# Kernel tuning notes

Hardware: AMD Instinct MI355X
Metric: run time of the kernel (lower is better)

Reference implementation:

```python
import jax, jax.numpy as jnp
import numpy as np

B, T, S, A = 4, 10, 6, 6
HID, L, IMG = 512, 6, 128
NCH = 16  # spatial-softmax channels
_px, _py = np.meshgrid(np.linspace(-1.0, 1.0, IMG), np.linspace(-1.0, 1.0, IMG))
POSX = jnp.asarray(_px.reshape(-1), jnp.float32)
POSY = jnp.asarray(_py.reshape(-1), jnp.float32)


def _conv_relu(x, w, b):
    y = jax.lax.conv_general_dilated(x, w, (1, 1), 'SAME',
                                     dimension_numbers=('NCHW', 'OIHW', 'NCHW'))
    return jax.nn.relu(y + b[None, :, None, None])


def _cnn_ss(x, ws, bs):
    for w, b in zip(ws, bs):
        x = _conv_relu(x, w, b)
    n = x.shape[0]
    attn = jax.nn.softmax(x.reshape(n, NCH, -1), axis=-1)  # (n, 16, H*W)
    ex = attn @ POSX  # (n, 16)
    ey = attn @ POSY
    return jnp.stack([ex, ey], axis=-1).reshape(n, 2 * NCH)  # (n, 32)


def _lstm_cell(x, h, c, wih, whh, bih, bhh):
    g = x @ wih.T + bih + h @ whh.T + bhh
    i, f, gg, o = jnp.split(g, 4, axis=-1)  # torch LSTMCell gate order i,f,g,o
    c2 = jax.nn.sigmoid(f) * c + jax.nn.sigmoid(i) * jnp.tanh(gg)
    h2 = jax.nn.sigmoid(o) * jnp.tanh(c2)
    return h2, c2


def setup_inputs() -> dict:
    key = jax.random.key(0)
    ks = iter(jax.random.split(key, 64))

    def nrm(shape, s=0.05):
        return jax.random.normal(next(ks), shape, dtype=jnp.float32) * s

    inp = {
        'seq_img_main': nrm((B, T, 3, IMG, IMG), 1.0),
        'seq_img_secondary': nrm((B, T, 3, IMG, IMG), 1.0),
        'seq_states': nrm((B, T, S), 1.0),
    }
    chans = [(32, 3), (64, 32), (128, 64), (16, 128)]
    for cam in ('m', 's'):
        for j, (o, ci) in enumerate(chans):
            inp[f'{cam}_w{j}'] = nrm((o, ci, 3, 3))
            inp[f'{cam}_b{j}'] = nrm((o,))
    in0, inr = S + 64, HID + 64  # 70 and 576
    inp['wih0'] = nrm((4 * HID, in0)); inp['whh0'] = nrm((4 * HID, HID))
    inp['bih0'] = nrm((4 * HID,)); inp['bhh0'] = nrm((4 * HID,))
    inp['wih_r'] = nrm((L - 1, 4 * HID, inr)); inp['whh_r'] = nrm((L - 1, 4 * HID, HID))
    inp['bih_r'] = nrm((L - 1, 4 * HID)); inp['bhh_r'] = nrm((L - 1, 4 * HID))
    inp['out_w'] = nrm((A, inr)); inp['out_b'] = nrm((A,))
    return inp


def reference(seq_img_main, seq_img_secondary, seq_states,
              m_w0, m_b0, m_w1, m_b1, m_w2, m_b2, m_w3, m_b3,
              s_w0, s_b0, s_w1, s_b1, s_w2, s_b2, s_w3, s_b3,
              wih0, whh0, bih0, bhh0, wih_r, whh_r, bih_r, bhh_r,
              out_w, out_b):
    b, t = seq_img_main.shape[:2]
    fm = _cnn_ss(seq_img_main.reshape(b * t, 3, IMG, IMG),
                 [m_w0, m_w1, m_w2, m_w3], [m_b0, m_b1, m_b2, m_b3])
    fs = _cnn_ss(seq_img_secondary.reshape(b * t, 3, IMG, IMG),
                 [s_w0, s_w1, s_w2, s_w3], [s_b0, s_b1, s_b2, s_b3])
    img = jnp.concatenate([fm, fs], axis=-1).reshape(b, t, 64)  # (B,T,64)

    h0 = jnp.zeros((L, b, HID), jnp.float32)
    c0 = jnp.zeros((L, b, HID), jnp.float32)

    def step(carry, xt):
        h, c = carry
        st, im = xt  # (B,S), (B,64)
        x = jnp.concatenate([st, im], axis=-1)
        hn, cn = _lstm_cell(x, h[0], c[0], wih0, whh0, bih0, bhh0)
        hs, cs = [hn], [cn]
        for l in range(L - 1):
            x = jnp.concatenate([hs[-1], im], axis=-1)
            hl, cl = _lstm_cell(x, h[l + 1], c[l + 1],
                                wih_r[l], whh_r[l], bih_r[l], bhh_r[l])
            hs.append(hl); cs.append(cl)
        out = jnp.concatenate([hs[-1], im], axis=-1) @ out_w.T + out_b
        return (jnp.stack(hs), jnp.stack(cs)), out

    _, outs = jax.lax.scan(step, (h0, c0),
                           (seq_states.transpose(1, 0, 2), img.transpose(1, 0, 2)))
    return outs.transpose(1, 0, 2)  # (B,T,A)
```

## Files before the change

### kernel.cpp

```cpp
#include <hip/hip_runtime.h>
#include <hip/hip_bf16.h>
#include <math.h>

typedef __hip_bfloat16 bf16;
typedef short bf16x8 __attribute__((ext_vector_type(8)));
typedef float f32x4 __attribute__((ext_vector_type(4)));

static constexpr int HWPX = 16384;

__device__ inline float sigmoidf_(float x) { return 1.0f / (1.0f + expf(-x)); }
__device__ inline float bflo(unsigned u) { return __uint_as_float(u << 16); }
__device__ inline float bfhi(unsigned u) { return __uint_as_float(u & 0xffff0000u); }
__device__ inline int swz(int x) { return (x ^ (x >> 2)) & 3; }

__device__ inline void gll16(const bf16* g, short* l) {
    __builtin_amdgcn_global_load_lds(
        (const __attribute__((address_space(1))) void*)g,
        (__attribute__((address_space(3))) void*)l, 16, 0, 0);
}

__global__ __launch_bounds__(256) void prep_lstm_k(
    const float* __restrict__ wih0, const float* __restrict__ whh0,
    const float* __restrict__ wihr, const float* __restrict__ whhr,
    bf16* __restrict__ d0, bf16* __restrict__ d1,
    bf16* __restrict__ d2, bf16* __restrict__ d3)
{
    const size_t nA = 2048ull * 72, nB = 2048ull * 512;
    const size_t nC = 5ull * 2048 * 576, nD = 5ull * 2048 * 512;
    for (size_t i = blockIdx.x * 256ull + threadIdx.x; i < nA + nB + nC + nD;
         i += (size_t)gridDim.x * 256) {
        if (i < nA) {
            int c = (int)(i % 72), r = (int)(i / 72);
            d0[i] = __float2bfloat16(c < 70 ? wih0[(size_t)r * 70 + c] : 0.f);
        } else if (i < nA + nB) {
            size_t k = i - nA; d1[k] = __float2bfloat16(whh0[k]);
        } else if (i < nA + nB + nC) {
            size_t k = i - nA - nB; d2[k] = __float2bfloat16(wihr[k]);
        } else {
            size_t k = i - nA - nB - nC; d3[k] = __float2bfloat16(whhr[k]);
        }
    }
}

struct ConvW {
    const float* src[8];
    bf16* dst[8];
};

__global__ __launch_bounds__(256) void prep_conv_k(ConvW a)
{
    const int sizes[4] = {3072, 18432, 73728, 18432};
    const int cins[4] = {3, 32, 64, 128};
    const int couts[4] = {32, 64, 128, 16};
    int total = 2 * 113664;
    for (int idx = blockIdx.x * 256 + threadIdx.x; idx < total; idx += gridDim.x * 256) {
        int i = idx, cam = 0;
        if (i >= 113664) { cam = 1; i -= 113664; }
        int layer = 0;
        while (layer < 3 && i >= sizes[layer]) { i -= sizes[layer]; ++layer; }
        const float* w = a.src[cam * 4 + layer];
        bf16* d = a.dst[cam * 4 + layer];
        if (layer == 0) {
            int k = i & 31, co = (i >> 5) & 31, ky = i >> 10;
            int kx = k >> 3, c = k & 7;
            float v = (kx < 3 && c < 3) ? w[((co * 3 + c) * 3 + ky) * 3 + kx] : 0.f;
            d[i] = __float2bfloat16(v);
        } else {
            int CIN = cins[layer], COUT = couts[layer], KC = CIN / 32;
            int e = i & 7;
            int t2 = i >> 3;
            int co = t2 % COUT;
            int t3 = t2 / COUT;
            int q = t3 & 3;
            int t4 = t3 >> 2;
            int kc = t4 % KC;
            int tap = t4 / KC;
            d[i] = __float2bfloat16(w[((size_t)(co * CIN + kc * 32 + q * 8 + e)) * 9 + tap]);
        }
    }
}

__global__ __launch_bounds__(256, 4) void conv01(
    const float* __restrict__ srcm, const float* __restrict__ srcs,
    const bf16* __restrict__ w0m, const bf16* __restrict__ w0s,
    const float* __restrict__ b0m, const float* __restrict__ b0s,
    const bf16* __restrict__ wTm, const bf16* __restrict__ wTs,
    const float* __restrict__ bm, const float* __restrict__ bs,
    bf16* __restrict__ out, int c0)
{
    constexpr int COUT = 64, MW = 2;
    constexpr int SLOTS = 4 * 264;

    const int y0 = (blockIdx.x >> 1) * 2;
    const int x0 = (blockIdx.x & 1) * 64;
    const int cam = blockIdx.y;
    const int img = blockIdx.z;
    const int ci_ = cam * gridDim.z + img;
    const float* inImg = (cam ? srcs : srcm) + (size_t)(c0 + img) * 3 * HWPX;
    const bf16* wT0 = cam ? w0s : w0m;
    const float* bias0 = cam ? b0s : b0m;
    const bf16* wT = cam ? wTs : wTm;
    const float* bias = cam ? bs : bm;
    const int tid = threadIdx.x;
    const int wave = tid >> 6, lane = tid & 63;
    const int wrow = wave >> 1, wm = wave & 1;
    const int q = lane >> 4, n16 = lane & 15;

    __shared__ short smem[SLOTS * 8];
    __shared__ short raw[6 * 68 * 16];

    for (int i = tid; i < SLOTS; i += 256)
        *(bf16x8*)(void*)&smem[i * 8] = (bf16x8)0;

    for (int d = tid; d < 6 * 68; d += 256) {
        int x = d % 68, r = d / 68;
        int yy = y0 - 2 + r, xx = x0 - 2 + x;
        bf16 v8[8];
#pragma unroll
        for (int c = 0; c < 8; ++c) v8[c] = __float2bfloat16(0.f);
        if ((unsigned)yy < 128u && (unsigned)xx < 128u) {
            int o = yy * 128 + xx;
            v8[0] = __float2bfloat16(inImg[o]);
            v8[1] = __float2bfloat16(inImg[HWPX + o]);
            v8[2] = __float2bfloat16(inImg[2 * HWPX + o]);
        }
        *(bf16x8*)(void*)&raw[d * 16] = *(bf16x8*)(void*)v8;
        *(bf16x8*)(void*)&raw[d * 16 + 8] = (bf16x8)0;
    }
    __syncthreads();

    const int co0_ = wm * 16 + n16;
    for (int rp = 0; rp < 4; ++rp) {
        int Y = y0 - 1 + rp;
        if ((unsigned)Y >= 128u) continue;
        for (int xg = wrow; xg < 5; xg += 2) {
            int xt = xg * 16 + n16;
            int xts = xt < 66 ? xt : 65;
            f32x4 a0 = f32x4{0.f, 0.f, 0.f, 0.f};
#pragma unroll
            for (int ky = 0; ky < 3; ++ky) {
                bf16x8 aF = *(const bf16x8*)(const void*)(wT0 +
                    ((size_t)(ky * 32 + co0_) * 32) + q * 8);
                int off = (q < 3) ? ((rp + ky) * 68 + xts + q) * 16
                                  : ((rp + ky) * 68 + xts) * 16 + 8;
                bf16x8 bF = *(const bf16x8*)(const void*)&raw[off];
                a0 = __builtin_amdgcn_mfma_f32_16x16x32_bf16(aF, bF, a0, 0, 0, 0);
            }
            int X = x0 - 1 + xt;
            if (xt < 66 && (unsigned)X < 128u) {
                int cb0 = wm * 16 + q * 4;
                bf16 tmp[4];
#pragma unroll
                for (int r = 0; r < 4; ++r) {
                    float v = a0[r] + bias0[cb0 + r];
                    tmp[r] = __float2bfloat16(v > 0.f ? v : 0.f);
                }
                int g = cb0 >> 3;
                int sbase = (rp * 264 + xt * 4 + (g ^ swz(xt))) * 8 + (q & 1) * 4;
                *reinterpret_cast<uint2*>(&smem[sbase]) = *reinterpret_cast<uint2*>(tmp);
            }
        }
    }
    __syncthreads();

    f32x4 acc[MW][4];
#pragma unroll
    for (int mt = 0; mt < MW; ++mt)
#pragma unroll
        for (int nt = 0; nt < 4; ++nt) acc[mt][nt] = f32x4{0.f, 0.f, 0.f, 0.f};

#pragma unroll
    for (int ky = 0; ky < 3; ++ky) {
#pragma unroll
        for (int kx = 0; kx < 3; ++kx) {
            bf16x8 aF[MW];
#pragma unroll
            for (int mt = 0; mt < MW; ++mt) {
                int co = (wm * MW + mt) * 16 + n16;
                aF[mt] = *(const bf16x8*)(const void*)(wT +
                    (((size_t)(ky * 3 + kx) * 4 + q) * COUT + co) * 8);
            }
#pragma unroll
            for (int nt = 0; nt < 4; ++nt) {
                int xt = nt * 16 + n16 + kx;
                int slot = (wrow + ky) * 264 + xt * 4 + (q ^ swz(xt));
                bf16x8 bF = *(const bf16x8*)(const void*)&smem[slot * 8];
#pragma unroll
                for (int mt = 0; mt < MW; ++mt)
                    acc[mt][nt] = __builtin_amdgcn_mfma_f32_16x16x32_bf16(
                        aF[mt], bF, acc[mt][nt], 0, 0, 0);
            }
        }
    }

    const int y = y0 + wrow;
#pragma unroll
    for (int mt = 0; mt < MW; ++mt) {
        int co0 = (wm * MW + mt) * 16 + q * 4;
#pragma unroll
        for (int nt = 0; nt < 4; ++nt) {
            int x = x0 + nt * 16 + n16;
            bf16 tmp[4];
#pragma unroll
            for (int r = 0; r < 4; ++r) {
                float v = acc[mt][nt][r] + bias[co0 + r];
                tmp[r] = __float2bfloat16(v > 0.f ? v : 0.f);
            }
            *reinterpret_cast<uint2*>(out + ((size_t)ci_ * HWPX + y * 128 + x) * COUT + co0)
                = *reinterpret_cast<uint2*>(tmp);
        }
    }
}

template <int CIN, int COUT>
__global__ __launch_bounds__(256, 4) void conv2r(
    const bf16* __restrict__ in, const bf16* __restrict__ wTm,
    const bf16* __restrict__ wTs, const float* __restrict__ bm,
    const float* __restrict__ bs, bf16* __restrict__ out,
    const char* __restrict__ zpage)
{
    constexpr int KC = CIN / 32;
    constexpr int NB = (KC > 1) ? 2 : 1;
    constexpr int MW = COUT / 32;
    constexpr int SLOTS = 4 * 264;

    const int y0 = (blockIdx.x >> 1) * 2;
    const int x0 = (blockIdx.x & 1) * 64;
    const int cam = blockIdx.y;
    const int img = blockIdx.z;
    const int ci_ = cam * gridDim.z + img;
    const bf16* wT = cam ? wTs : wTm;
    const float* bias = cam ? bs : bm;
    const int tid = threadIdx.x;
    const int wave = tid >> 6, lane = tid & 63;
    const int wrow = wave >> 1, wm = wave & 1;
    const int q = lane >> 4, n16 = lane & 15;

    __shared__ short smem[NB][SLOTS * 8];
    const bf16* inImg = in + (size_t)ci_ * HWPX * CIN;

    const bf16* sptr[5];
#pragma unroll
    for (int it = 0; it < 5; ++it) {
        int s = it * 256 + tid;
        int r = s / 264, s2 = s - r * 264;
        int sx = s2 >> 2;
        int g = (s2 & 3) ^ swz(sx);
        int yy = y0 + r - 1, xx = x0 + sx - 1;
        bool ok = (s < SLOTS) && ((unsigned)yy < 128u) && ((unsigned)xx < 128u);
        sptr[it] = ok ? inImg + ((size_t)yy * 128 + xx) * CIN + g * 8
                      : (const bf16*)(zpage + (tid & 255) * 16);
    }
    auto stage = [&](int kc, int buf) {
#pragma unroll
        for (int it = 0; it < 5; ++it) {
            if (it * 256 + tid < SLOTS)
                gll16(sptr[it] + kc * 32, &smem[buf][it * 2048 + wave * 512]);
        }
    };

    f32x4 acc[MW][4];
#pragma unroll
    for (int mt = 0; mt < MW; ++mt)
#pragma unroll
        for (int nt = 0; nt < 4; ++nt) acc[mt][nt] = f32x4{0.f, 0.f, 0.f, 0.f};

    stage(0, 0);
    for (int kc = 0; kc < KC; ++kc) {
        __syncthreads();
        if (kc + 1 < KC) stage(kc + 1, (kc + 1) % NB);
        const short* sb = smem[kc % NB];
#pragma unroll
        for (int ky = 0; ky < 3; ++ky) {
#pragma unroll
            for (int kx = 0; kx < 3; ++kx) {
                bf16x8 aF[MW];
#pragma unroll
                for (int mt = 0; mt < MW; ++mt) {
                    int co = (wm * MW + mt) * 16 + n16;
                    aF[mt] = *(const bf16x8*)(const void*)(wT +
                        ((((size_t)(ky * 3 + kx) * KC + kc) * 4 + q) * COUT + co) * 8);
                }
#pragma unroll
                for (int nt = 0; nt < 4; ++nt) {
                    int xt = nt * 16 + n16 + kx;
                    int slot = (wrow + ky) * 264 + xt * 4 + (q ^ swz(xt));
                    bf16x8 bF = *(const bf16x8*)(const void*)&sb[slot * 8];
#pragma unroll
                    for (int mt = 0; mt < MW; ++mt)
                        acc[mt][nt] = __builtin_amdgcn_mfma_f32_16x16x32_bf16(
                            aF[mt], bF, acc[mt][nt], 0, 0, 0);
                }
            }
        }
    }

    const int y = y0 + wrow;
#pragma unroll
    for (int mt = 0; mt < MW; ++mt) {
        int co0 = (wm * MW + mt) * 16 + q * 4;
#pragma unroll
        for (int nt = 0; nt < 4; ++nt) {
            int x = x0 + nt * 16 + n16;
            bf16 tmp[4];
#pragma unroll
            for (int r = 0; r < 4; ++r) {
                float v = acc[mt][nt][r] + bias[co0 + r];
                tmp[r] = __float2bfloat16(v > 0.f ? v : 0.f);
            }
            *reinterpret_cast<uint2*>(out + ((size_t)ci_ * HWPX + y * 128 + x) * COUT + co0)
                = *reinterpret_cast<uint2*>(tmp);
        }
    }
}

__global__ __launch_bounds__(256, 2) void conv4_r4(
    const bf16* __restrict__ in, const bf16* __restrict__ wTm,
    const bf16* __restrict__ wTs, const float* __restrict__ bm,
    const float* __restrict__ bs,
    float* __restrict__ partial,
    const char* __restrict__ zpage, int c0)
{
    constexpr int CIN = 128, KC = 4;
    constexpr int RR = 4;
    constexpr int SLOTS = (RR + 2) * 264;
    const int y0 = (blockIdx.x >> 1) * RR;
    const int xh = blockIdx.x & 1;
    const int x0 = xh * 64;
    const int cam = blockIdx.y;
    const int img = blockIdx.z;
    const int ci_ = cam * gridDim.z + img;
    const int gimg = cam * 40 + c0 + img;
    const bf16* wT = cam ? wTs : wTm;
    const float* bias = cam ? bs : bm;
    const int tid = threadIdx.x;
    const int wave = tid >> 6, lane = tid & 63;
    const int q = lane >> 4, n16 = lane & 15;

    __shared__ short smem[2][SLOTS * 8];
    __shared__ float sred[3][RR][4][16];
    const bf16* inImg = in + (size_t)ci_ * HWPX * CIN;

    const bf16* sptr[7];
#pragma unroll
    for (int it = 0; it < 7; ++it) {
        int s = it * 256 + tid;
        int r = s / 264, s2 = s - r * 264;
        int sx = s2 >> 2;
        int g = (s2 & 3) ^ swz(sx);
        int yy = y0 + r - 1, xx = x0 + sx - 1;
        bool ok = (s < SLOTS) && ((unsigned)yy < 128u) && ((unsigned)xx < 128u);
        sptr[it] = ok ? inImg + ((size_t)yy * 128 + xx) * CIN + g * 8
                      : (const bf16*)(zpage + (tid & 255) * 16);
    }
    auto stage = [&](int kc, int buf) {
#pragma unroll
        for (int it = 0; it < 7; ++it) {
            if (it * 256 + tid < SLOTS)
                gll16(sptr[it] + kc * 32, &smem[buf][it * 2048 + wave * 512]);
        }
    };

    f32x4 acc[RR];
#pragma unroll
    for (int rp = 0; rp < RR; ++rp) acc[rp] = f32x4{0.f, 0.f, 0.f, 0.f};

    stage(0, 0);
    for (int kc = 0; kc < KC; ++kc) {
        __syncthreads();
        if (kc + 1 < KC) stage(kc + 1, (kc + 1) & 1);
        const short* sb = smem[kc & 1];
#pragma unroll
        for (int ky = 0; ky < 3; ++ky) {
#pragma unroll
            for (int kx = 0; kx < 3; ++kx) {
                bf16x8 aF = *(const bf16x8*)(const void*)(wT +
                    ((((size_t)(ky * 3 + kx) * KC + kc) * 4 + q) * 16 + n16) * 8);
                int xt = wave * 16 + n16 + kx;
                int sbase = xt * 4 + (q ^ swz(xt));
#pragma unroll
                for (int rp = 0; rp < RR; ++rp) {
                    bf16x8 bF = *(const bf16x8*)(const void*)
                        &sb[((rp + ky) * 264 + sbase) * 8];
                    acc[rp] = __builtin_amdgcn_mfma_f32_16x16x32_bf16(
                        aF, bF, acc[rp], 0, 0, 0);
                }
            }
        }
    }

    int x = x0 + wave * 16 + n16;
    float px = -1.f + (2.f / 127.f) * x;
    float v[RR][4], M[RR][4];
#pragma unroll
    for (int rp = 0; rp < RR; ++rp)
#pragma unroll
        for (int r = 0; r < 4; ++r) {
            float t = acc[rp][r] + bias[q * 4 + r];
            v[rp][r] = t > 0.f ? t : 0.f;
            M[rp][r] = v[rp][r];
        }
#pragma unroll
    for (int rp = 0; rp < RR; ++rp)
#pragma unroll
        for (int r = 0; r < 4; ++r) {
            M[rp][r] = fmaxf(M[rp][r], __shfl_xor(M[rp][r], 1));
            M[rp][r] = fmaxf(M[rp][r], __shfl_xor(M[rp][r], 2));
            M[rp][r] = fmaxf(M[rp][r], __shfl_xor(M[rp][r], 4));
            M[rp][r] = fmaxf(M[rp][r], __shfl_xor(M[rp][r], 8));
        }
    if (n16 == 0)
#pragma unroll
        for (int rp = 0; rp < RR; ++rp)
#pragma unroll
            for (int r = 0; r < 4; ++r) sred[0][rp][wave][q * 4 + r] = M[rp][r];
    __syncthreads();
#pragma unroll
    for (int rp = 0; rp < RR; ++rp)
#pragma unroll
        for (int r = 0; r < 4; ++r) {
            M[rp][r] = fmaxf(fmaxf(sred[0][rp][0][q * 4 + r], sred[0][rp][1][q * 4 + r]),
                             fmaxf(sred[0][rp][2][q * 4 + r], sred[0][rp][3][q * 4 + r]));
        }
    float s[RR][4], sx[RR][4];
#pragma unroll
    for (int rp = 0; rp < RR; ++rp)
#pragma unroll
        for (int r = 0; r < 4; ++r) {
            float e = expf(v[rp][r] - M[rp][r]);
            s[rp][r] = e; sx[rp][r] = e * px;
            s[rp][r] += __shfl_xor(s[rp][r], 1);  sx[rp][r] += __shfl_xor(sx[rp][r], 1);
            s[rp][r] += __shfl_xor(s[rp][r], 2);  sx[rp][r] += __shfl_xor(sx[rp][r], 2);
            s[rp][r] += __shfl_xor(s[rp][r], 4);  sx[rp][r] += __shfl_xor(sx[rp][r], 4);
            s[rp][r] += __shfl_xor(s[rp][r], 8);  sx[rp][r] += __shfl_xor(sx[rp][r], 8);
        }
    __syncthreads();
    if (n16 == 0)
#pragma unroll
        for (int rp = 0; rp < RR; ++rp)
#pragma unroll
            for (int r = 0; r < 4; ++r) {
                sred[1][rp][wave][q * 4 + r] = s[rp][r];
                sred[2][rp][wave][q * 4 + r] = sx[rp][r];
            }
    __syncthreads();
    if (tid < 16 * RR) {
        int rp = tid >> 4, c = tid & 15;
        float S = sred[1][rp][0][c] + sred[1][rp][1][c] + sred[1][rp][2][c] + sred[1][rp][3][c];
        float SX = sred[2][rp][0][c] + sred[2][rp][1][c] + sred[2][rp][2][c] + sred[2][rp][3][c];
        float Mv = fmaxf(fmaxf(sred[0][rp][0][c], sred[0][rp][1][c]),
                         fmaxf(sred[0][rp][2][c], sred[0][rp][3][c]));
        float* pp = partial + (((size_t)gimg * 16 + c) * 256 + ((y0 + rp) * 2 + xh)) * 4;
        pp[0] = Mv; pp[1] = S; pp[2] = SX;
    }
}

__global__ __launch_bounds__(256) void ssmerge_k(
    const float* __restrict__ partial, float* __restrict__ featm,
    float* __restrict__ feats)
{
    const int img = blockIdx.x;
    const int cam = img / 40, li = img % 40;
    float* feat = cam ? feats : featm;
    const int tid = threadIdx.x;
    const int co = tid >> 4, s = tid & 15;
    const float* base = partial + ((size_t)img * 16 + co) * 256 * 4;
    float M = -1e30f, S = 0.f, SX = 0.f, SY = 0.f;
    for (int i = s; i < 256; i += 16) {
        float m = base[i * 4], sv = base[i * 4 + 1], sxv = base[i * 4 + 2];
        float py = -1.f + (2.f / 127.f) * (i >> 1);
        float Mn = fmaxf(M, m);
        float w0 = expf(M - Mn), w1 = expf(m - Mn);
        S = S * w0 + sv * w1;
        SX = SX * w0 + sxv * w1;
        SY = SY * w0 + sv * py * w1;
        M = Mn;
    }
#pragma unroll
    for (int mask = 1; mask < 16; mask <<= 1) {
        float Mo = __shfl_xor(M, mask), So = __shfl_xor(S, mask);
        float SXo = __shfl_xor(SX, mask), SYo = __shfl_xor(SY, mask);
        float Mn = fmaxf(M, Mo);
        float w0 = expf(M - Mn), w1 = expf(Mo - Mn);
        S = S * w0 + So * w1; SX = SX * w0 + SXo * w1; SY = SY * w0 + SYo * w1;
        M = Mn;
    }
    if (s == 0) {
        feat[(size_t)li * 32 + 2 * co] = SX / S;
        feat[(size_t)li * 32 + 2 * co + 1] = SY / S;
    }
}

__device__ inline float imgfeat(const float* featm, const float* feats,
                                int b, int t, int k)
{
    int idx = (b * 10 + t) * 32;
    return k < 32 ? featm[idx + k] : feats[idx + k - 32];
}

template <int NB1>
__device__ inline void cell_mm(const bf16* __restrict__ wih,
                               const bf16* __restrict__ whh,
                               const float* __restrict__ xs0,
                               int j, int sub, float (&dg)[4][4])
{
    constexpr int K1 = NB1 * 8;
    constexpr int XS = K1 + 512;
#pragma unroll
    for (int r = 0; r < 4; ++r) {
        const uint4* __restrict__ w1 =
            reinterpret_cast<const uint4*>(wih + (size_t)(j + r * 512) * K1);
#pragma unroll
        for (int g0 = 0; g0 < NB1; g0 += 8) {
            int g = g0 + sub;
            if (g0 + 7 < NB1 || g < NB1) {
                uint4 u = w1[g];
                float a0 = bflo(u.x), a1 = bfhi(u.x), a2 = bflo(u.y), a3 = bfhi(u.y);
                float a4 = bflo(u.z), a5 = bfhi(u.z), a6 = bflo(u.w), a7 = bfhi(u.w);
#pragma unroll
                for (int b = 0; b < 4; ++b) {
                    const float* xp = xs0 + b * XS + g * 8;
                    dg[r][b] += a0 * xp[0] + a1 * xp[1] + a2 * xp[2] + a3 * xp[3]
                              + a4 * xp[4] + a5 * xp[5] + a6 * xp[6] + a7 * xp[7];
                }
            }
        }
        const uint4* __restrict__ w2 =
            reinterpret_cast<const uint4*>(whh + (size_t)(j + r * 512) * 512);
#pragma unroll
        for (int gi = 0; gi < 8; ++gi) {
            int g = gi * 8 + sub;
            uint4 u = w2[g];
            float a0 = bflo(u.x), a1 = bfhi(u.x), a2 = bflo(u.y), a3 = bfhi(u.y);
            float a4 = bflo(u.z), a5 = bfhi(u.z), a6 = bflo(u.w), a7 = bfhi(u.w);
#pragma unroll
            for (int b = 0; b < 4; ++b) {
                const float* xp = xs0 + b * XS + K1 + g * 8;
                dg[r][b] += a0 * xp[0] + a1 * xp[1] + a2 * xp[2] + a3 * xp[3]
                          + a4 * xp[4] + a5 * xp[5] + a6 * xp[6] + a7 * xp[7];
            }
        }
    }
}

template <int NB1>
__device__ inline void cell_step(
    int l, int t, int bx,
    const bf16* __restrict__ wih, const bf16* __restrict__ whh,
    const float* __restrict__ bih, const float* __restrict__ bhh,
    const float* __restrict__ states,
    const float* __restrict__ featm, const float* __restrict__ feats,
    float* __restrict__ hAll, float* __restrict__ cst,
    float* __restrict__ xs)
{
    constexpr int K1 = NB1 * 8;
    constexpr int XS = K1 + 512;
    const int tid = threadIdx.x;
    const int jloc = tid >> 3;
    const int sub = tid & 7;
    const int j = bx * 32 + jloc;

    const float* hprev = (l == 0) ? nullptr
                       : hAll + ((size_t)(t + 1) * 6 + (l - 1)) * 2048;
    const float* hold  = hAll + ((size_t)t * 6 + l) * 2048;
    float* hnew        = hAll + ((size_t)(t + 1) * 6 + l) * 2048;

    if (NB1 == 72) {
        for (int i = tid; i < 4 * 512; i += 256) {
            int bb = i >> 9, kk = i & 511;
            float2 cv;
            int base;
            if (kk < 256) {
                cv = *reinterpret_cast<const float2*>(&hprev[bb * 512 + kk * 2]);
                base = bb * XS + kk * 2;
            } else {
                cv = *reinterpret_cast<const float2*>(&hold[bb * 512 + (kk - 256) * 2]);
                base = bb * XS + 576 + (kk - 256) * 2;
            }
            xs[base] = cv.x; xs[base + 1] = cv.y;
        }
        {
            int bb = tid >> 6, k = tid & 63;
            xs[bb * XS + 512 + k] = imgfeat(featm, feats, bb, t, k);
        }
    } else {
        for (int i = tid; i < 4 * 256; i += 256) {
            int bb = i >> 8, kk = i & 255;
            float2 cv = *reinterpret_cast<const float2*>(&hold[bb * 512 + kk * 2]);
            int base = bb * XS + 72 + kk * 2;
            xs[base] = cv.x; xs[base + 1] = cv.y;
        }
        for (int i = tid; i < 4 * 72; i += 256) {
            int bb = i / 72, k = i - bb * 72;
            float v = (k < 6) ? states[(bb * 10 + t) * 6 + k]
                              : (k < 70 ? imgfeat(featm, feats, bb, t, k - 6) : 0.f);
            xs[bb * XS + k] = v;
        }
    }
    __syncthreads();

    float dg[4][4] = {{0.f, 0.f, 0.f, 0.f}, {0.f, 0.f, 0.f, 0.f},
                      {0.f, 0.f, 0.f, 0.f}, {0.f, 0.f, 0.f, 0.f}};
    cell_mm<NB1>(wih, whh, xs, j, sub, dg);

#pragma unroll
    for (int r = 0; r < 4; ++r)
#pragma unroll
        for (int b = 0; b < 4; ++b) {
            dg[r][b] += __shfl_xor(dg[r][b], 1);
            dg[r][b] += __shfl_xor(dg[r][b], 2);
            dg[r][b] += __shfl_xor(dg[r][b], 4);
        }

    if (sub == 0) {
        float b0 = bih[j] + bhh[j];
        float b1 = bih[j + 512] + bhh[j + 512];
        float b2 = bih[j + 1024] + bhh[j + 1024];
        float b3 = bih[j + 1536] + bhh[j + 1536];
#pragma unroll
        for (int b = 0; b < 4; ++b) {
            float gi = dg[0][b] + b0;
            float gf = dg[1][b] + b1;
            float gg = dg[2][b] + b2;
            float go = dg[3][b] + b3;
            float cp = cst[b * 512 + j];
            float c2 = sigmoidf_(gf) * cp + sigmoidf_(gi) * tanhf(gg);
            float h2 = sigmoidf_(go) * tanhf(c2);
            cst[b * 512 + j] = c2;
            hnew[b * 512 + j] = h2;
        }
    }
}

__global__ __launch_bounds__(256) void lstm_diag2_k(
    const bf16* __restrict__ wih0p, const bf16* __restrict__ whh0b,
    const bf16* __restrict__ wihrb, const bf16* __restrict__ whhrb,
    const float* __restrict__ bih0, const float* __restrict__ bhh0,
    const float* __restrict__ bihr, const float* __restrict__ bhhr,
    const float* __restrict__ states,
    const float* __restrict__ featm, const float* __restrict__ feats,
    float* __restrict__ hAll, float* __restrict__ cAll,
    const float* __restrict__ out_w, const float* __restrict__ out_b,
    float* __restrict__ out, int d)
{
    const int l = blockIdx.y;
    const int bx = blockIdx.x;
    const int tid = threadIdx.x;
    __shared__ float xs[4 * 1088];

    if (l == 6) {
        int t = d - 6;
        if (t < 0 || t >= 10 || bx != 0) return;
        const float* h5 = hAll + ((size_t)(t + 1) * 6 + 5) * 2048;
        int p = tid >> 3, sub = tid & 7;
        if (p >= 24) return;
        int b = p / 6, a = p % 6;
        const float* wr = out_w + a * 576;
        float acc = 0.f;
        for (int k = sub; k < 256; k += 8) {
            float2 cv = *reinterpret_cast<const float2*>(&h5[b * 512 + k * 2]);
            acc += wr[k * 2] * cv.x + wr[k * 2 + 1] * cv.y;
        }
        for (int k = sub; k < 64; k += 8)
            acc += wr[512 + k] * imgfeat(featm, feats, b, t, k);
        acc += __shfl_xor(acc, 1);
        acc += __shfl_xor(acc, 2);
        acc += __shfl_xor(acc, 4);
        if (sub == 0) out[(b * 10 + t) * 6 + a] = acc + out_b[a];
        return;
    }

    const int t = d - l;
    if (t < 0 || t >= 10) return;

    float* cst = cAll + (size_t)l * 2048;
    if (l == 0) {
        cell_step<9>(0, t, bx, wih0p, whh0b, bih0, bhh0,
                     states, featm, feats, hAll, cst, xs);
    } else {
        const bf16* wih = wihrb + (size_t)(l - 1) * 2048 * 576;
        const bf16* whh = whhrb + (size_t)(l - 1) * 2048 * 512;
        const float* bih = bihr + (l - 1) * 2048;
        const float* bhh = bhhr + (l - 1) * 2048;
        cell_step<72>(l, t, bx, wih, whh, bih, bhh,
                      states, featm, feats, hAll, cst, xs);
    }
}

extern "C" void kernel_launch(void* const* d_in, const int* in_sizes, int n_in,
                              void* d_out, int out_size, void* d_ws, size_t ws_size,
                              hipStream_t stream)
{
    const float* seq_m = (const float*)d_in[0];
    const float* seq_s = (const float*)d_in[1];
    const float* states = (const float*)d_in[2];
    const float *cw[2][4], *cb[2][4];
    for (int cam = 0; cam < 2; ++cam)
        for (int j = 0; j < 4; ++j) {
            cw[cam][j] = (const float*)d_in[3 + cam * 8 + j * 2];
            cb[cam][j] = (const float*)d_in[3 + cam * 8 + j * 2 + 1];
        }
    const float* wih0  = (const float*)d_in[19];
    const float* whh0  = (const float*)d_in[20];
    const float* bih0  = (const float*)d_in[21];
    const float* bhh0  = (const float*)d_in[22];
    const float* wih_r = (const float*)d_in[23];
    const float* whh_r = (const float*)d_in[24];
    const float* bih_r = (const float*)d_in[25];
    const float* bhh_r = (const float*)d_in[26];
    const float* out_w = (const float*)d_in[27];
    const float* out_b = (const float*)d_in[28];
    float* out = (float*)d_out;

    char* wsc = (char*)d_ws;
    auto carve = [&](size_t bytes) {
        char* p = wsc;
        wsc += (bytes + 255) & ~(size_t)255;
        return p;
    };
    float* featm = (float*)carve(40 * 32 * 4);
    float* feats = (float*)carve(40 * 32 * 4);
    float* hAll  = (float*)carve((size_t)11 * 6 * 2048 * 4);
    float* cAll  = (float*)carve((size_t)6 * 2048 * 4);
    char*  zpage = carve(8192);
    float* partial = (float*)carve((size_t)80 * 16 * 256 * 4 * 4);
    const int wtElts[4] = {3072, 18432, 73728, 18432};
    bf16* wT[2][4];
    for (int cam = 0; cam < 2; ++cam)
        for (int j = 0; j < 4; ++j) wT[cam][j] = (bf16*)carve(wtElts[j] * 2);
    bf16* wih0p = (bf16*)carve((size_t)2048 * 72 * 2);
    bf16* whh0b = (bf16*)carve((size_t)2048 * 512 * 2);
    bf16* wihrb = (bf16*)carve((size_t)5 * 2048 * 576 * 2);
    bf16* whhrb = (bf16*)carve((size_t)5 * 2048 * 512 * 2);

    size_t used = (size_t)(wsc - (char*)d_ws);
    size_t rem = ws_size > used ? ws_size - used : 0;
    int CHI = 1;
    const int cands[8] = {40, 20, 10, 8, 5, 4, 2, 1};
    for (int i = 0; i < 8; ++i) {
        size_t need = (size_t)2 * cands[i] * (128 + 64) * HWPX * 2;
        if (need <= rem) { CHI = cands[i]; break; }
    }
    bf16* bufA = (bf16*)carve((size_t)2 * CHI * HWPX * 128 * 2);
    bf16* bufB = (bf16*)carve((size_t)2 * CHI * HWPX * 64 * 2);

    hipMemsetAsync(hAll, 0, 6 * 2048 * 4, stream);
    hipMemsetAsync(cAll, 0, 6 * 2048 * 4, stream);
    hipMemsetAsync(zpage, 0, 8192, stream);

    prep_lstm_k<<<2048, 256, 0, stream>>>(wih0, whh0, wih_r, whh_r,
                                          wih0p, whh0b, wihrb, whhrb);
    ConvW cwArg;
    for (int cam = 0; cam < 2; ++cam)
        for (int j = 0; j < 4; ++j) {
            cwArg.src[cam * 4 + j] = cw[cam][j];
            cwArg.dst[cam * 4 + j] = wT[cam][j];
        }
    prep_conv_k<<<888, 256, 0, stream>>>(cwArg);

    for (int c0 = 0; c0 < 40; c0 += CHI) {
        int ch = (40 - c0) < CHI ? (40 - c0) : CHI;
        conv01<<<dim3(128, 2, ch), 256, 0, stream>>>(
            seq_m, seq_s, wT[0][0], wT[1][0], cb[0][0], cb[1][0],
            wT[0][1], wT[1][1], cb[0][1], cb[1][1], bufB, c0);
        conv2r<64, 128><<<dim3(128, 2, ch), 256, 0, stream>>>(
            bufB, wT[0][2], wT[1][2], cb[0][2], cb[1][2], bufA, zpage);
        conv4_r4<<<dim3(64, 2, ch), 256, 0, stream>>>(
            bufA, wT[0][3], wT[1][3], cb[0][3], cb[1][3], partial, zpage, c0);
    }
    ssmerge_k<<<80, 256, 0, stream>>>(partial, featm, feats);

    for (int d = 0; d < 16; ++d) {
        lstm_diag2_k<<<dim3(16, 7), 256, 0, stream>>>(
            wih0p, whh0b, wihrb, whhrb, bih0, bhh0, bih_r, bhh_r,
            states, featm, feats, hAll, cAll, out_w, out_b, out, d);
    }
}
```

Baseline: 1.113 ms.

## Merge prep kernels and memsets, restructure conv01 layer-0 wave mapping

```diff
diff --git a/kernel.cpp b/kernel.cpp
--- a/kernel.cpp
+++ b/kernel.cpp
@@ -19,68 +19,67 @@
         (__attribute__((address_space(3))) void*)l, 16, 0, 0);
 }
 
-__global__ __launch_bounds__(256) void prep_lstm_k(
-    const float* __restrict__ wih0, const float* __restrict__ whh0,
-    const float* __restrict__ wihr, const float* __restrict__ whhr,
-    bf16* __restrict__ d0, bf16* __restrict__ d1,
-    bf16* __restrict__ d2, bf16* __restrict__ d3)
-{
-    const size_t nA = 2048ull * 72, nB = 2048ull * 512;
-    const size_t nC = 5ull * 2048 * 576, nD = 5ull * 2048 * 512;
-    for (size_t i = blockIdx.x * 256ull + threadIdx.x; i < nA + nB + nC + nD;
-         i += (size_t)gridDim.x * 256) {
-        if (i < nA) {
-            int c = (int)(i % 72), r = (int)(i / 72);
-            d0[i] = __float2bfloat16(c < 70 ? wih0[(size_t)r * 70 + c] : 0.f);
-        } else if (i < nA + nB) {
-            size_t k = i - nA; d1[k] = __float2bfloat16(whh0[k]);
-        } else if (i < nA + nB + nC) {
-            size_t k = i - nA - nB; d2[k] = __float2bfloat16(wihr[k]);
-        } else {
-            size_t k = i - nA - nB - nC; d3[k] = __float2bfloat16(whhr[k]);
-        }
-    }
-}
-
 struct ConvW {
     const float* src[8];
     bf16* dst[8];
 };
 
-__global__ __launch_bounds__(256) void prep_conv_k(ConvW a)
-{
+__global__ __launch_bounds__(256) void prep_all_k(
+    const float* __restrict__ wih0, const float* __restrict__ whh0,
+    const float* __restrict__ wihr, const float* __restrict__ whhr,
+    bf16* __restrict__ d0, bf16* __restrict__ d1,
+    bf16* __restrict__ d2, bf16* __restrict__ d3, ConvW a)
+{
+    const size_t nA = 2048ull * 72, nB = 2048ull * 512;
+    const size_t nC = 5ull * 2048 * 576, nD = 5ull * 2048 * 512;
+    const size_t nLstm = nA + nB + nC + nD;
+    const size_t nConv = 2 * 113664;
     const int sizes[4] = {3072, 18432, 73728, 18432};
     const int cins[4] = {3, 32, 64, 128};
     const int couts[4] = {32, 64, 128, 16};
-    int total = 2 * 113664;
-    for (int idx = blockIdx.x * 256 + threadIdx.x; idx < total; idx += gridDim.x * 256) {
-        int i = idx, cam = 0;
-        if (i >= 113664) { cam = 1; i -= 113664; }
-        int layer = 0;
-        while (layer < 3 && i >= sizes[layer]) { i -= sizes[layer]; ++layer; }
-        const float* w = a.src[cam * 4 + layer];
-        bf16* d = a.dst[cam * 4 + layer];
-        if (layer == 0) {
-            int k = i & 31, co = (i >> 5) & 31, ky = i >> 10;
-            int kx = k >> 3, c = k & 7;
-            float v = (kx < 3 && c < 3) ? w[((co * 3 + c) * 3 + ky) * 3 + kx] : 0.f;
-            d[i] = __float2bfloat16(v);
+
+    for (size_t i = blockIdx.x * 256ull + threadIdx.x; i < nLstm + nConv;
+         i += (size_t)gridDim.x * 256) {
+        if (i < nLstm) {
+            if (i < nA) {
+                int c = (int)(i % 72), r = (int)(i / 72);
+                d0[i] = __float2bfloat16(c < 70 ? wih0[(size_t)r * 70 + c] : 0.f);
+            } else if (i < nA + nB) {
+                size_t k = i - nA; d1[k] = __float2bfloat16(whh0[k]);
+            } else if (i < nA + nB + nC) {
+                size_t k = i - nA - nB; d2[k] = __float2bfloat16(wihr[k]);
+            } else {
+                size_t k = i - nA - nB - nC; d3[k] = __float2bfloat16(whhr[k]);
+            }
         } else {
-            int CIN = cins[layer], COUT = couts[layer], KC = CIN / 32;
-            int e = i & 7;
-            int t2 = i >> 3;
-            int co = t2 % COUT;
-            int t3 = t2 / COUT;
-            int q = t3 & 3;
-            int t4 = t3 >> 2;
-            int kc = t4 % KC;
-            int tap = t4 / KC;
-            d[i] = __float2bfloat16(w[((size_t)(co * CIN + kc * 32 + q * 8 + e)) * 9 + tap]);
-        }
-    }
-}
-
-__global__ __launch_bounds__(256, 4) void conv01(
+            int ci = (int)(i - nLstm), cam = 0;
+            if (ci >= 113664) { cam = 1; ci -= 113664; }
+            int layer = 0;
+            while (layer < 3 && ci >= sizes[layer]) { ci -= sizes[layer]; ++layer; }
+            const float* w = a.src[cam * 4 + layer];
+            bf16* d = a.dst[cam * 4 + layer];
+            if (layer == 0) {
+                int k = ci & 31, co = (ci >> 5) & 31, ky = ci >> 10;
+                int kx = k >> 3, c = k & 7;
+                float v = (kx < 3 && c < 3) ? w[((co * 3 + c) * 3 + ky) * 3 + kx] : 0.f;
+                d[ci] = __float2bfloat16(v);
+            } else {
+                int CIN = cins[layer], COUT = couts[layer], KC = CIN / 32;
+                int e = ci & 7;
+                int t2 = ci >> 3;
+                int co = t2 % COUT;
+                int t3 = t2 / COUT;
+                int q = t3 & 3;
+                int t4 = t3 >> 2;
+                int kc = t4 % KC;
+                int tap = t4 / KC;
+                d[ci] = __float2bfloat16(w[((size_t)(co * CIN + kc * 32 + q * 8 + e)) * 9 + tap]);
+            }
+        }
+    }
+}
+
+__global__ __launch_bounds__(256, 5) void conv01(
     const float* __restrict__ srcm, const float* __restrict__ srcs,
     const bf16* __restrict__ w0m, const bf16* __restrict__ w0s,
     const float* __restrict__ b0m, const float* __restrict__ b0s,
@@ -109,9 +108,6 @@
     __shared__ short smem[SLOTS * 8];
     __shared__ short raw[6 * 68 * 16];
 
-    for (int i = tid; i < SLOTS; i += 256)
-        *(bf16x8*)(void*)&smem[i * 8] = (bf16x8)0;
-
     for (int d = tid; d < 6 * 68; d += 256) {
         int x = d % 68, r = d / 68;
         int yy = y0 - 2 + r, xx = x0 - 2 + x;
@@ -129,35 +125,43 @@
     }
     __syncthreads();
 
-    const int co0_ = wm * 16 + n16;
-    for (int rp = 0; rp < 4; ++rp) {
-        int Y = y0 - 1 + rp;
-        if ((unsigned)Y >= 128u) continue;
-        for (int xg = wrow; xg < 5; xg += 2) {
+    {
+        const int rp = wave;
+        const int Y = y0 - 1 + rp;
+        const bool yok = (unsigned)Y < 128u;
+        for (int xg = 0; xg < 5; ++xg) {
             int xt = xg * 16 + n16;
             int xts = xt < 66 ? xt : 65;
-            f32x4 a0 = f32x4{0.f, 0.f, 0.f, 0.f};
-#pragma unroll
-            for (int ky = 0; ky < 3; ++ky) {
-                bf16x8 aF = *(const bf16x8*)(const void*)(wT0 +
-                    ((size_t)(ky * 32 + co0_) * 32) + q * 8);
-                int off = (q < 3) ? ((rp + ky) * 68 + xts + q) * 16
-                                  : ((rp + ky) * 68 + xts) * 16 + 8;
-                bf16x8 bF = *(const bf16x8*)(const void*)&raw[off];
-                a0 = __builtin_amdgcn_mfma_f32_16x16x32_bf16(aF, bF, a0, 0, 0, 0);
-            }
-            int X = x0 - 1 + xt;
-            if (xt < 66 && (unsigned)X < 128u) {
-                int cb0 = wm * 16 + q * 4;
-                bf16 tmp[4];
-#pragma unroll
-                for (int r = 0; r < 4; ++r) {
-                    float v = a0[r] + bias0[cb0 + r];
-                    tmp[r] = __float2bfloat16(v > 0.f ? v : 0.f);
+#pragma unroll
+            for (int coH = 0; coH < 2; ++coH) {
+                f32x4 a0 = f32x4{0.f, 0.f, 0.f, 0.f};
+#pragma unroll
+                for (int ky = 0; ky < 3; ++ky) {
+                    bf16x8 aF = *(const bf16x8*)(const void*)(wT0 +
+                        ((size_t)(ky * 32 + coH * 16 + n16) * 32) + q * 8);
+                    int off = (q < 3) ? ((rp + ky) * 68 + xts + q) * 16
+                                      : ((rp + ky) * 68 + xts) * 16 + 8;
+                    bf16x8 bF = *(const bf16x8*)(const void*)&raw[off];
+                    a0 = __builtin_amdgcn_mfma_f32_16x16x32_bf16(aF, bF, a0, 0, 0, 0);
                 }
-                int g = cb0 >> 3;
-                int sbase = (rp * 264 + xt * 4 + (g ^ swz(xt))) * 8 + (q & 1) * 4;
-                *reinterpret_cast<uint2*>(&smem[sbase]) = *reinterpret_cast<uint2*>(tmp);
+                if (xt < 66) {
+                    int X = x0 - 1 + xt;
+                    bool ok = yok && (unsigned)X < 128u;
+                    int cb0 = coH * 16 + q * 4;
+                    bf16 tmp[4];
+#pragma unroll
+                    for (int r = 0; r < 4; ++r) {
+                        float v = 0.f;
+                        if (ok) {
+                            v = a0[r] + bias0[cb0 + r];
+                            v = v > 0.f ? v : 0.f;
+                        }
+                        tmp[r] = __float2bfloat16(v);
+                    }
+                    int g = cb0 >> 3;
+                    int sbase = (rp * 264 + xt * 4 + (g ^ swz(xt))) * 8 + (q & 1) * 4;
+                    *reinterpret_cast<uint2*>(&smem[sbase]) = *reinterpret_cast<uint2*>(tmp);
+                }
             }
         }
     }
@@ -720,9 +724,9 @@
     };
     float* featm = (float*)carve(40 * 32 * 4);
     float* feats = (float*)carve(40 * 32 * 4);
-    float* hAll  = (float*)carve((size_t)11 * 6 * 2048 * 4);
     float* cAll  = (float*)carve((size_t)6 * 2048 * 4);
     char*  zpage = carve(8192);
+    float* hAll  = (float*)carve((size_t)11 * 6 * 2048 * 4);
     float* partial = (float*)carve((size_t)80 * 16 * 256 * 4 * 4);
     const int wtElts[4] = {3072, 18432, 73728, 18432};
     bf16* wT[2][4];
@@ -744,19 +748,16 @@
     bf16* bufA = (bf16*)carve((size_t)2 * CHI * HWPX * 128 * 2);
     bf16* bufB = (bf16*)carve((size_t)2 * CHI * HWPX * 64 * 2);
 
-    hipMemsetAsync(hAll, 0, 6 * 2048 * 4, stream);
-    hipMemsetAsync(cAll, 0, 6 * 2048 * 4, stream);
-    hipMemsetAsync(zpage, 0, 8192, stream);
-
-    prep_lstm_k<<<2048, 256, 0, stream>>>(wih0, whh0, wih_r, whh_r,
-                                          wih0p, whh0b, wihrb, whhrb);
+    hipMemsetAsync(cAll, 0, 49152 + 8192 + 49152, stream);
+
     ConvW cwArg;
     for (int cam = 0; cam < 2; ++cam)
         for (int j = 0; j < 4; ++j) {
             cwArg.src[cam * 4 + j] = cw[cam][j];
             cwArg.dst[cam * 4 + j] = wT[cam][j];
         }
-    prep_conv_k<<<888, 256, 0, stream>>>(cwArg);
+    prep_all_k<<<2048, 256, 0, stream>>>(wih0, whh0, wih_r, whh_r,
+                                         wih0p, whh0b, wihrb, whhrb, cwArg);
 
     for (int c0 = 0; c0 < 40; c0 += CHI) {
         int ch = (40 - c0) < CHI ? (40 - c0) : CHI;
```

After: 1.075 ms. 1.04x faster.
